# Optimization experiments

Measured on AMD Instinct MI355X. Metric: run time of the kernel, lower is better.

## Reference

```python
import jax, jax.numpy as jnp
import numpy as np

B, S, D = 2, 2048, 1024
N_HEADS = 16
HEAD_DIM = D // N_HEADS
D_FF = 4 * D
EPS = 1e-5


def setup_inputs() -> dict:
    key = jax.random.key(0)
    ks = jax.random.split(key, 16)
    s = 0.02
    return {
        "x": jax.random.normal(ks[0], (B, S, D), dtype=jnp.float32),
        "ln1_scale": jnp.ones((D,), jnp.float32),
        "ln1_shift": jnp.zeros((D,), jnp.float32),
        "wq": jax.random.normal(ks[1], (D, D), jnp.float32) * s,
        "wk": jax.random.normal(ks[2], (D, D), jnp.float32) * s,
        "wv": jax.random.normal(ks[3], (D, D), jnp.float32) * s,
        "wo": jax.random.normal(ks[4], (D, D), jnp.float32) * s,
        "bo": jnp.zeros((D,), jnp.float32),
        "ln2_scale": jnp.ones((D,), jnp.float32),
        "ln2_shift": jnp.zeros((D,), jnp.float32),
        "w1": jax.random.normal(ks[5], (D, D_FF), jnp.float32) * s,
        "b1": jnp.zeros((D_FF,), jnp.float32),
        "w2": jax.random.normal(ks[6], (D_FF, D), jnp.float32) * s,
        "b2": jnp.zeros((D,), jnp.float32),
    }


def _layer_norm(x, scale, shift):
    mean = jnp.mean(x, axis=-1, keepdims=True)
    var = jnp.var(x, axis=-1, keepdims=True)  # unbiased=False
    return (x - mean) / jnp.sqrt(var + EPS) * scale + shift


def _mha(x, wq, wk, wv, wo, bo):
    b, s, d = x.shape
    q = (x @ wq).reshape(b, s, N_HEADS, HEAD_DIM).transpose(0, 2, 1, 3)
    k = (x @ wk).reshape(b, s, N_HEADS, HEAD_DIM).transpose(0, 2, 1, 3)
    v = (x @ wv).reshape(b, s, N_HEADS, HEAD_DIM).transpose(0, 2, 1, 3)
    scores = jnp.einsum('bhqd,bhkd->bhqk', q, k)
    causal = jnp.tril(jnp.ones((s, s), dtype=bool))  # mask upper triangle
    scores = jnp.where(causal, scores, -jnp.inf)
    attn = jax.nn.softmax(scores / np.sqrt(HEAD_DIM).astype(np.float32), axis=-1)
    ctx = jnp.einsum('bhqk,bhkd->bhqd', attn, v)
    ctx = ctx.transpose(0, 2, 1, 3).reshape(b, s, d)
    return ctx @ wo + bo


def reference(x, ln1_scale, ln1_shift, wq, wk, wv, wo, bo,
              ln2_scale, ln2_shift, w1, b1, w2, b2):
    # Attention sub-block (dropout is identity in eval / droprate=0)
    h = x + _mha(_layer_norm(x, ln1_scale, ln1_shift), wq, wk, wv, wo, bo)
    # FFN sub-block (note: original code discards the dropout(inp) result and
    # returns shortcut + ff_output, which is the standard residual)
    y = _layer_norm(h, ln2_scale, ln2_shift)
    ff = jax.nn.gelu(y @ w1 + b1, approximate=True) @ w2 + b2
    return h + ff
```

## Files before the change

kernel.cpp:

```cpp
#include <hip/hip_runtime.h>
#include <hip/hip_bf16.h>

typedef unsigned short u16;
typedef unsigned int u32;
typedef __bf16 bf16x8 __attribute__((ext_vector_type(8)));
typedef float f32x4 __attribute__((ext_vector_type(4)));

#if __has_builtin(__builtin_amdgcn_exp2f)
#define FEXP2 __builtin_amdgcn_exp2f
#else
#define FEXP2 exp2f
#endif

#if __has_builtin(__builtin_amdgcn_rcpf)
#define FRCP __builtin_amdgcn_rcpf
#else
#define FRCP(x) (1.0f / (x))
#endif

#define QSCALE 0.1803368801f

__device__ __forceinline__ u16 f2bf(float f) {
  __hip_bfloat16 h = __float2bfloat16(f);
  return __builtin_bit_cast(u16, h);
}

__device__ __forceinline__ u32 pack2_bf16(float a, float b) {
  u32 ua = __builtin_bit_cast(u32, a);
  ua += 0x7FFFu + ((ua >> 16) & 1u);
  u32 ub = __builtin_bit_cast(u32, b);
  ub += 0x7FFFu + ((ub >> 16) & 1u);
  return (ua >> 16) | (ub & 0xFFFF0000u);
}

__device__ __forceinline__ void load_lds16(const u16* g, u16* l) {
  __builtin_amdgcn_global_load_lds((const __attribute__((address_space(1))) void*)g,
                                   (__attribute__((address_space(3))) void*)l, 16, 0, 0);
}

__global__ __launch_bounds__(256) void tconv_kernel(const float* __restrict__ src,
                                                    u16* __restrict__ dst, int R, int C) {
  __shared__ float tile[32][33];
  int bx = blockIdx.x * 32, by = blockIdx.y * 32;
  int tx = threadIdx.x, ty = threadIdx.y;
#pragma unroll
  for (int i = 0; i < 4; ++i)
    tile[ty + 8 * i][tx] = src[(size_t)(by + ty + 8 * i) * C + bx + tx];
  __syncthreads();
#pragma unroll
  for (int i = 0; i < 4; ++i)
    dst[(size_t)(bx + ty + 8 * i) * R + by + tx] = f2bf(tile[tx][ty + 8 * i]);
}

__global__ __launch_bounds__(256) void ln_kernel(const float* __restrict__ src,
                                                 u16* __restrict__ dst,
                                                 const float* __restrict__ gamma,
                                                 const float* __restrict__ beta) {
  int row = blockIdx.x, tid = threadIdx.x;
  const float4 v = ((const float4*)(src + (size_t)row * 1024))[tid];
  float s = v.x + v.y + v.z + v.w;
  float q = v.x * v.x + v.y * v.y + v.z * v.z + v.w * v.w;
#pragma unroll
  for (int off = 32; off >= 1; off >>= 1) {
    s += __shfl_down(s, off, 64);
    q += __shfl_down(q, off, 64);
  }
  __shared__ float red[8];
  if ((tid & 63) == 0) { red[(tid >> 6) * 2] = s; red[(tid >> 6) * 2 + 1] = q; }
  __syncthreads();
  s = red[0] + red[2] + red[4] + red[6];
  q = red[1] + red[3] + red[5] + red[7];
  float mean = s * (1.0f / 1024.0f);
  float var = q * (1.0f / 1024.0f) - mean * mean;
  float rstd = rsqrtf(var + 1e-5f);
  float4 g = ((const float4*)gamma)[tid];
  float4 b = ((const float4*)beta)[tid];
  ushort4 o;
  o.x = f2bf((v.x - mean) * rstd * g.x + b.x);
  o.y = f2bf((v.y - mean) * rstd * g.y + b.y);
  o.z = f2bf((v.z - mean) * rstd * g.z + b.z);
  o.w = f2bf((v.w - mean) * rstd * g.w + b.w);
  *(ushort4*)(dst + (size_t)row * 1024 + tid * 4) = o;
}

template <int MODE>
__device__ __forceinline__ void epilogue_elem(float v, int row, int col, int N,
                                              const float* __restrict__ bias,
                                              const float* __restrict__ resid,
                                              void* __restrict__ outp,
                                              void* __restrict__ outp2,
                                              void* __restrict__ outp3) {
  if constexpr (MODE == 0) {
    const int slotc = col >> 6;
    const int ty = slotc >> 4;
    const int h = slotc & 15, d = col & 63;
    const int bb = row >> 11, s = row & 2047;
    if (ty == 0) {
      ((u16*)outp)[(((size_t)(bb * 16 + h)) * 2048 + s) * 64 + d] = f2bf(v * QSCALE);
    } else if (ty == 1) {
      ((u16*)outp2)[(((size_t)(bb * 16 + h)) * 2048 + s) * 64 + d] = f2bf(v);
    } else {
      const int spos = (s & ~31) | ((s & 15) << 1) | ((s >> 4) & 1);
      ((u16*)outp3)[(((size_t)(bb * 16 + h)) * 64 + d) * 2048 + spos] = f2bf(v);
    }
  } else if constexpr (MODE == 3) {
    ((float*)outp)[(size_t)row * N + col] = v + bias[col] + resid[(size_t)row * N + col];
  } else if constexpr (MODE == 4) {
    float u = v + bias[col];
    float c = u * (0.7978845608f + 0.0356774081f * u * u);
    float t = FEXP2(c * -2.885390082f);
    ((u16*)outp)[(size_t)row * N + col] = f2bf(u * FRCP(1.0f + t));
  } else if constexpr (MODE == 5) {
    ((float*)outp)[(size_t)row * N + col] = v + bias[col] + resid[(size_t)row * N + col];
  }
}

template <int MODE, int BN>
__global__ __launch_bounds__(256, 2) void gemm2(const u16* __restrict__ A,
                                                const u16* __restrict__ BT,
                                                int M, int N, int K, int nbx,
                                                const float* __restrict__ bias,
                                                const float* __restrict__ resid,
                                                void* __restrict__ outp,
                                                void* __restrict__ outp2,
                                                void* __restrict__ outp3) {
  constexpr int NJ = BN / 32;
  const int tid = threadIdx.x, lane = tid & 63, wave = tid >> 6;
  const int l16 = lane & 15, quad = lane >> 4;
  const int id = blockIdx.x, xcd = id & 7, s = id >> 3;
  const int by = xcd * 4 + s / nbx, bx = s - (s / nbx) * nbx;
  const int mblk = by * 128, nblk = bx * BN;
  const int m0w = (wave >> 1) * 64, n0w = (wave & 1) * (BN / 2);

  __shared__ u16 Ab[2][128 * 32];
  __shared__ u16 Bb[2][BN * 32];

  f32x4 acc[4][NJ];
#pragma unroll
  for (int i = 0; i < 4; ++i)
#pragma unroll
    for (int j = 0; j < NJ; ++j)
#pragma unroll
      for (int r = 0; r < 4; ++r) acc[i][j][r] = 0.0f;

  const int srow = lane >> 2, schunk = lane & 3;
  const u16* gA = A + (size_t)(mblk + wave * 32 + srow) * K + schunk * 8;
  u16* lA0 = Ab[0] + (wave * 32) * 32;
  u16* lA1 = Ab[1] + (wave * 32) * 32;
  const int bwrows = (BN == 128) ? wave * 32 : wave * 16;
  const u16* gB = BT + (size_t)(nblk + bwrows + srow) * K + schunk * 8;
  u16* lB0 = Bb[0] + bwrows * 32;
  u16* lB1 = Bb[1] + bwrows * 32;

  for (int k0 = 0; k0 < K; k0 += 64) {
    __syncthreads();
    load_lds16(gA + k0, lA0);
    load_lds16(gA + 16 * (size_t)K + k0, lA0 + 16 * 32);
    load_lds16(gA + k0 + 32, lA1);
    load_lds16(gA + 16 * (size_t)K + k0 + 32, lA1 + 16 * 32);
    if constexpr (BN == 128) {
      load_lds16(gB + k0, lB0);
      load_lds16(gB + 16 * (size_t)K + k0, lB0 + 16 * 32);
      load_lds16(gB + k0 + 32, lB1);
      load_lds16(gB + 16 * (size_t)K + k0 + 32, lB1 + 16 * 32);
    } else {
      load_lds16(gB + k0, lB0);
      load_lds16(gB + k0 + 32, lB1);
    }
    asm volatile("s_waitcnt vmcnt(0)" ::: "memory");
    __syncthreads();

#pragma unroll
    for (int h = 0; h < 2; ++h) {
      bf16x8 af[4], bfr[NJ];
#pragma unroll
      for (int i = 0; i < 4; ++i)
        af[i] = *(const bf16x8*)(Ab[h] + (m0w + i * 16 + l16) * 32 + quad * 8);
#pragma unroll
      for (int j = 0; j < NJ; ++j)
        bfr[j] = *(const bf16x8*)(Bb[h] + (n0w + j * 16 + l16) * 32 + quad * 8);
#pragma unroll
      for (int i = 0; i < 4; ++i)
#pragma unroll
        for (int j = 0; j < NJ; ++j)
          acc[i][j] = __builtin_amdgcn_mfma_f32_16x16x32_bf16(af[i], bfr[j], acc[i][j], 0, 0, 0);
    }
  }

#pragma unroll
  for (int i = 0; i < 4; ++i)
#pragma unroll
    for (int j = 0; j < NJ; ++j) {
      const int col = nblk + n0w + j * 16 + l16;
#pragma unroll
      for (int r = 0; r < 4; ++r)
        epilogue_elem<MODE>(acc[i][j][r], mblk + m0w + i * 16 + quad * 4 + r, col, N,
                            bias, resid, outp, outp2, outp3);
    }
}

__global__ __launch_bounds__(256) void attn_kernel(const u16* __restrict__ Q,
                                                   const u16* __restrict__ Kb,
                                                   const u16* __restrict__ VT,
                                                   u16* __restrict__ ctx) {
  const int tid = threadIdx.x, lane = tid & 63, wave = tid >> 6;
  const int l16 = lane & 15, quad = lane >> 4;
  const int id = blockIdx.x, xcd = id & 7, slot = id >> 3;
  const int bh = xcd + 8 * (slot & 3);
  const int pr = slot >> 2;
  const int qt = (wave < 2) ? (31 - pr) : pr;
  const int b = bh >> 4, hh = bh & 15;
  const int q0 = qt * 64 + (wave & 1) * 32;

  const u16* qp = Q + (size_t)bh * 2048 * 64;
  const u16* kp = Kb + (size_t)bh * 2048 * 64;
  const u16* vp = VT + (size_t)bh * 64 * 2048;

  bf16x8 qf[2][2];
#pragma unroll
  for (int rf = 0; rf < 2; ++rf)
#pragma unroll
    for (int kk = 0; kk < 2; ++kk)
      qf[rf][kk] = *(const bf16x8*)(qp + (size_t)(q0 + rf * 16 + l16) * 64 + kk * 32 + quad * 8);

  f32x4 o[2][4], lac[2];
#pragma unroll
  for (int rf = 0; rf < 2; ++rf) {
#pragma unroll
    for (int r = 0; r < 4; ++r) lac[rf][r] = 0.0f;
#pragma unroll
    for (int dt = 0; dt < 4; ++dt)
#pragma unroll
      for (int r = 0; r < 4; ++r) o[rf][dt][r] = 0.0f;
  }

  bf16x8 onef;
#pragma unroll
  for (int i = 0; i < 8; ++i) onef[i] = (__bf16)1.0f;

  __shared__ u16 pbuf[4][32 * 40];
  u16* pw = pbuf[wave];

  const int nfull = q0 >> 5;

  bf16x8 kf[2][2], vf[4], kfn[2][2], vfn[4];
#pragma unroll
  for (int st = 0; st < 2; ++st)
#pragma unroll
    for (int kk = 0; kk < 2; ++kk)
      kf[st][kk] = *(const bf16x8*)(kp + (size_t)(st * 16 + l16) * 64 + kk * 32 + quad * 8);
#pragma unroll
  for (int dt = 0; dt < 4; ++dt)
    vf[dt] = *(const bf16x8*)(vp + (size_t)(dt * 16 + l16) * 2048 + quad * 8);

  for (int kt = 0; kt <= nfull; ++kt) {
    const int kb0 = kt * 32;
    f32x4 sc[2][2];
#pragma unroll
    for (int rf = 0; rf < 2; ++rf)
#pragma unroll
      for (int st = 0; st < 2; ++st) {
#pragma unroll
        for (int r = 0; r < 4; ++r) sc[rf][st][r] = 0.0f;
#pragma unroll
        for (int kk = 0; kk < 2; ++kk)
          sc[rf][st] = __builtin_amdgcn_mfma_f32_16x16x32_bf16(qf[rf][kk], kf[st][kk], sc[rf][st], 0, 0, 0);
      }

    const int kbn = (kt < nfull) ? kb0 + 32 : 0;
#pragma unroll
    for (int st = 0; st < 2; ++st)
#pragma unroll
      for (int kk = 0; kk < 2; ++kk)
        kfn[st][kk] = *(const bf16x8*)(kp + (size_t)(kbn + st * 16 + l16) * 64 + kk * 32 + quad * 8);
#pragma unroll
    for (int dt = 0; dt < 4; ++dt)
      vfn[dt] = *(const bf16x8*)(vp + (size_t)(dt * 16 + l16) * 2048 + kbn + quad * 8);

    const bool masked = (kt == nfull);
#pragma unroll
    for (int rf = 0; rf < 2; ++rf)
#pragma unroll
      for (int r = 0; r < 4; ++r) {
        float s0 = sc[rf][0][r], s1 = sc[rf][1][r];
        if (masked) {
          const int rel = rf * 16 + quad * 4 + r;
          if (l16 > rel) s0 = -INFINITY;
          if (16 + l16 > rel) s1 = -INFINITY;
        }
        *(u32*)(pw + (rf * 16 + quad * 4 + r) * 40 + l16 * 2) =
            pack2_bf16(FEXP2(s0), FEXP2(s1));
      }
    asm volatile("s_waitcnt lgkmcnt(0)" ::: "memory");
#pragma unroll
    for (int rf = 0; rf < 2; ++rf) {
      bf16x8 pf = *(const bf16x8*)(pw + (rf * 16 + l16) * 40 + quad * 8);
      lac[rf] = __builtin_amdgcn_mfma_f32_16x16x32_bf16(pf, onef, lac[rf], 0, 0, 0);
#pragma unroll
      for (int dt = 0; dt < 4; ++dt)
        o[rf][dt] = __builtin_amdgcn_mfma_f32_16x16x32_bf16(pf, vf[dt], o[rf][dt], 0, 0, 0);
    }
#pragma unroll
    for (int st = 0; st < 2; ++st)
#pragma unroll
      for (int kk = 0; kk < 2; ++kk) kf[st][kk] = kfn[st][kk];
#pragma unroll
    for (int dt = 0; dt < 4; ++dt) vf[dt] = vfn[dt];
  }

#pragma unroll
  for (int rf = 0; rf < 2; ++rf)
#pragma unroll
    for (int r = 0; r < 4; ++r) {
      const float inv = 1.0f / lac[rf][r];
      const int row = q0 + rf * 16 + quad * 4 + r;
#pragma unroll
      for (int dt = 0; dt < 4; ++dt) {
        const int col = dt * 16 + l16;
        ctx[((size_t)(b * 2048 + row)) * 1024 + hh * 64 + col] = f2bf(o[rf][dt][r] * inv);
      }
    }
}

extern "C" void kernel_launch(void* const* d_in, const int* in_sizes, int n_in,
                              void* d_out, int out_size, void* d_ws, size_t ws_size,
                              hipStream_t stream) {
  (void)in_sizes; (void)n_in; (void)out_size; (void)ws_size;
  const float* x    = (const float*)d_in[0];
  const float* g1   = (const float*)d_in[1];
  const float* s1   = (const float*)d_in[2];
  const float* wq   = (const float*)d_in[3];
  const float* wk   = (const float*)d_in[4];
  const float* wv   = (const float*)d_in[5];
  const float* wo   = (const float*)d_in[6];
  const float* bo   = (const float*)d_in[7];
  const float* g2   = (const float*)d_in[8];
  const float* s2   = (const float*)d_in[9];
  const float* w1   = (const float*)d_in[10];
  const float* b1   = (const float*)d_in[11];
  const float* w2   = (const float*)d_in[12];
  const float* b2   = (const float*)d_in[13];

  char* ws = (char*)d_ws;
  u16* wqkvT = (u16*)(ws + 0);
  u16* woT   = (u16*)(ws + 6291456);
  u16* w1T   = (u16*)(ws + 8388608);
  u16* w2T   = (u16*)(ws + 16777216);
  u16* xn    = (u16*)(ws + 25165824);
  u16* qb    = (u16*)(ws + 33554432);
  u16* kb    = (u16*)(ws + 41943040);
  u16* vT    = (u16*)(ws + 50331648);
  u16* ctx   = (u16*)(ws + 58720256);
  u16* f     = (u16*)(ws + 33554432);
  float* h   = (float*)(ws + 67108864);
  u16* y     = xn;

  dim3 tb(32, 8);
  tconv_kernel<<<dim3(32, 32), tb, 0, stream>>>(wq, wqkvT, 1024, 1024);
  tconv_kernel<<<dim3(32, 32), tb, 0, stream>>>(wk, wqkvT + 1024 * 1024, 1024, 1024);
  tconv_kernel<<<dim3(32, 32), tb, 0, stream>>>(wv, wqkvT + 2048 * 1024, 1024, 1024);
  tconv_kernel<<<dim3(32, 32), tb, 0, stream>>>(wo, woT, 1024, 1024);
  tconv_kernel<<<dim3(128, 32), tb, 0, stream>>>(w1, w1T, 1024, 4096);
  tconv_kernel<<<dim3(32, 128), tb, 0, stream>>>(w2, w2T, 4096, 1024);

  ln_kernel<<<4096, 256, 0, stream>>>(x, xn, g1, s1);

  gemm2<0, 128><<<768, 256, 0, stream>>>(xn, wqkvT, 4096, 3072, 1024, 24,
                                         nullptr, nullptr, qb, kb, vT);

  attn_kernel<<<512, 256, 0, stream>>>(qb, kb, vT, ctx);

  gemm2<3, 64><<<512, 256, 0, stream>>>(ctx, woT, 4096, 1024, 1024, 16, bo, x, h,
                                        nullptr, nullptr);

  ln_kernel<<<4096, 256, 0, stream>>>(h, y, g2, s2);

  gemm2<4, 128><<<1024, 256, 0, stream>>>(y, w1T, 4096, 4096, 1024, 32,
                                          b1, nullptr, f, nullptr, nullptr);
  gemm2<5, 64><<<512, 256, 0, stream>>>(f, w2T, 4096, 1024, 4096, 16, b2, h,
                                        (float*)d_out, nullptr, nullptr);
}
```

Measured before the change: 365.8 us.

## Halve attention query rows per wave and double the grid

Each attention wave now processes 16 query rows instead of 32, with the work pairing remapped so the grid grows to 1024 blocks and launch bounds request higher occupancy. Per-wave register and LDS footprint shrinks, which should improve latency hiding and load balance across CUs. In exchange, each K/V fragment loaded from global memory is reused across half as many query rows, doubling K/V load traffic per unit of compute.

```diff
diff --git a/kernel.cpp b/kernel.cpp
--- a/kernel.cpp
+++ b/kernel.cpp
@@ -199,46 +199,42 @@
     }
 }
 
-__global__ __launch_bounds__(256) void attn_kernel(const u16* __restrict__ Q,
-                                                   const u16* __restrict__ Kb,
-                                                   const u16* __restrict__ VT,
-                                                   u16* __restrict__ ctx) {
+__global__ __launch_bounds__(256, 4) void attn_kernel(const u16* __restrict__ Q,
+                                                      const u16* __restrict__ Kb,
+                                                      const u16* __restrict__ VT,
+                                                      u16* __restrict__ ctx) {
   const int tid = threadIdx.x, lane = tid & 63, wave = tid >> 6;
   const int l16 = lane & 15, quad = lane >> 4;
   const int id = blockIdx.x, xcd = id & 7, slot = id >> 3;
   const int bh = xcd + 8 * (slot & 3);
   const int pr = slot >> 2;
-  const int qt = (wave < 2) ? (31 - pr) : pr;
+  const int w01 = wave & 1;
+  const int qw = (wave < 2) ? (127 - 2 * pr - w01) : (2 * pr + w01);
   const int b = bh >> 4, hh = bh & 15;
-  const int q0 = qt * 64 + (wave & 1) * 32;
+  const int q0 = qw * 16;
 
   const u16* qp = Q + (size_t)bh * 2048 * 64;
   const u16* kp = Kb + (size_t)bh * 2048 * 64;
   const u16* vp = VT + (size_t)bh * 64 * 2048;
 
-  bf16x8 qf[2][2];
-#pragma unroll
-  for (int rf = 0; rf < 2; ++rf)
-#pragma unroll
-    for (int kk = 0; kk < 2; ++kk)
-      qf[rf][kk] = *(const bf16x8*)(qp + (size_t)(q0 + rf * 16 + l16) * 64 + kk * 32 + quad * 8);
-
-  f32x4 o[2][4], lac[2];
-#pragma unroll
-  for (int rf = 0; rf < 2; ++rf) {
-#pragma unroll
-    for (int r = 0; r < 4; ++r) lac[rf][r] = 0.0f;
-#pragma unroll
-    for (int dt = 0; dt < 4; ++dt)
-#pragma unroll
-      for (int r = 0; r < 4; ++r) o[rf][dt][r] = 0.0f;
-  }
+  bf16x8 qf[2];
+#pragma unroll
+  for (int kk = 0; kk < 2; ++kk)
+    qf[kk] = *(const bf16x8*)(qp + (size_t)(q0 + l16) * 64 + kk * 32 + quad * 8);
+
+  f32x4 o[4], lac;
+#pragma unroll
+  for (int r = 0; r < 4; ++r) lac[r] = 0.0f;
+#pragma unroll
+  for (int dt = 0; dt < 4; ++dt)
+#pragma unroll
+    for (int r = 0; r < 4; ++r) o[dt][r] = 0.0f;
 
   bf16x8 onef;
 #pragma unroll
   for (int i = 0; i < 8; ++i) onef[i] = (__bf16)1.0f;
 
-  __shared__ u16 pbuf[4][32 * 40];
+  __shared__ u16 pbuf[4][16 * 40];
   u16* pw = pbuf[wave];
 
   const int nfull = q0 >> 5;
@@ -255,17 +251,15 @@
 
   for (int kt = 0; kt <= nfull; ++kt) {
     const int kb0 = kt * 32;
-    f32x4 sc[2][2];
-#pragma unroll
-    for (int rf = 0; rf < 2; ++rf)
-#pragma unroll
-      for (int st = 0; st < 2; ++st) {
-#pragma unroll
-        for (int r = 0; r < 4; ++r) sc[rf][st][r] = 0.0f;
-#pragma unroll
-        for (int kk = 0; kk < 2; ++kk)
-          sc[rf][st] = __builtin_amdgcn_mfma_f32_16x16x32_bf16(qf[rf][kk], kf[st][kk], sc[rf][st], 0, 0, 0);
-      }
+    f32x4 sc[2];
+#pragma unroll
+    for (int st = 0; st < 2; ++st) {
+#pragma unroll
+      for (int r = 0; r < 4; ++r) sc[st][r] = 0.0f;
+#pragma unroll
+      for (int kk = 0; kk < 2; ++kk)
+        sc[st] = __builtin_amdgcn_mfma_f32_16x16x32_bf16(qf[kk], kf[st][kk], sc[st], 0, 0, 0);
+    }
 
     const int kbn = (kt < nfull) ? kb0 + 32 : 0;
 #pragma unroll
@@ -279,27 +273,21 @@
 
     const bool masked = (kt == nfull);
 #pragma unroll
-    for (int rf = 0; rf < 2; ++rf)
-#pragma unroll
-      for (int r = 0; r < 4; ++r) {
-        float s0 = sc[rf][0][r], s1 = sc[rf][1][r];
-        if (masked) {
-          const int rel = rf * 16 + quad * 4 + r;
-          if (l16 > rel) s0 = -INFINITY;
-          if (16 + l16 > rel) s1 = -INFINITY;
-        }
-        *(u32*)(pw + (rf * 16 + quad * 4 + r) * 40 + l16 * 2) =
-            pack2_bf16(FEXP2(s0), FEXP2(s1));
+    for (int r = 0; r < 4; ++r) {
+      float s0 = sc[0][r], s1 = sc[1][r];
+      if (masked) {
+        const int rel = q0 - kb0 + quad * 4 + r;
+        if (l16 > rel) s0 = -INFINITY;
+        if (16 + l16 > rel) s1 = -INFINITY;
       }
+      *(u32*)(pw + (quad * 4 + r) * 40 + l16 * 2) = pack2_bf16(FEXP2(s0), FEXP2(s1));
+    }
     asm volatile("s_waitcnt lgkmcnt(0)" ::: "memory");
-#pragma unroll
-    for (int rf = 0; rf < 2; ++rf) {
-      bf16x8 pf = *(const bf16x8*)(pw + (rf * 16 + l16) * 40 + quad * 8);
-      lac[rf] = __builtin_amdgcn_mfma_f32_16x16x32_bf16(pf, onef, lac[rf], 0, 0, 0);
-#pragma unroll
-      for (int dt = 0; dt < 4; ++dt)
-        o[rf][dt] = __builtin_amdgcn_mfma_f32_16x16x32_bf16(pf, vf[dt], o[rf][dt], 0, 0, 0);
-    }
+    bf16x8 pf = *(const bf16x8*)(pw + l16 * 40 + quad * 8);
+    lac = __builtin_amdgcn_mfma_f32_16x16x32_bf16(pf, onef, lac, 0, 0, 0);
+#pragma unroll
+    for (int dt = 0; dt < 4; ++dt)
+      o[dt] = __builtin_amdgcn_mfma_f32_16x16x32_bf16(pf, vf[dt], o[dt], 0, 0, 0);
 #pragma unroll
     for (int st = 0; st < 2; ++st)
 #pragma unroll
@@ -309,17 +297,15 @@
   }
 
 #pragma unroll
-  for (int rf = 0; rf < 2; ++rf)
-#pragma unroll
-    for (int r = 0; r < 4; ++r) {
-      const float inv = 1.0f / lac[rf][r];
-      const int row = q0 + rf * 16 + quad * 4 + r;
-#pragma unroll
-      for (int dt = 0; dt < 4; ++dt) {
-        const int col = dt * 16 + l16;
-        ctx[((size_t)(b * 2048 + row)) * 1024 + hh * 64 + col] = f2bf(o[rf][dt][r] * inv);
-      }
-    }
+  for (int r = 0; r < 4; ++r) {
+    const float inv = 1.0f / lac[r];
+    const int row = q0 + quad * 4 + r;
+#pragma unroll
+    for (int dt = 0; dt < 4; ++dt) {
+      const int col = dt * 16 + l16;
+      ctx[((size_t)(b * 2048 + row)) * 1024 + hh * 64 + col] = f2bf(o[dt][r] * inv);
+    }
+  }
 }
 
 extern "C" void kernel_launch(void* const* d_in, const int* in_sizes, int n_in,
@@ -368,7 +354,7 @@
   gemm2<0, 128><<<768, 256, 0, stream>>>(xn, wqkvT, 4096, 3072, 1024, 24,
                                          nullptr, nullptr, qb, kb, vT);
 
-  attn_kernel<<<512, 256, 0, stream>>>(qb, kb, vT, ctx);
+  attn_kernel<<<1024, 256, 0, stream>>>(qb, kb, vT, ctx);
 
   gemm2<3, 64><<<512, 256, 0, stream>>>(ctx, woT, 4096, 1024, 1024, 16, bo, x, h,
                                         nullptr, nullptr);
```

Result: slower. 416.7 us (+13.9%).
